# Kernel tuning notes

Measured on AMD Instinct MI355X. Metric: run time of the kernel, lower is better.

The kernel has to match this reference:

```python
import jax, jax.numpy as jnp
import numpy as np

N_NODES = 50000
N_EDGES = 800000
F_IN = 64
F_OUT = 64


def setup_inputs() -> dict:
    key = jax.random.key(0)
    k1, k2, k3, k4, k5 = jax.random.split(key, 5)
    x = jax.random.normal(k1, (N_NODES, F_IN), dtype=jnp.float32)
    edge_index = jax.random.randint(k2, (2, N_EDGES), 0, N_NODES, dtype=jnp.int32)
    # PyG GraphConv params: lin_rel (with bias) applied to aggregated neighbors,
    # lin_root (no bias) applied to the node's own features.
    scale = 1.0 / np.sqrt(F_IN)
    W_rel = jax.random.uniform(k3, (F_OUT, F_IN), dtype=jnp.float32, minval=-scale, maxval=scale)
    b_rel = jax.random.uniform(k4, (F_OUT,), dtype=jnp.float32, minval=-scale, maxval=scale)
    W_root = jax.random.uniform(k5, (F_OUT, F_IN), dtype=jnp.float32, minval=-scale, maxval=scale)
    return {"x": x, "W_rel": W_rel, "b_rel": b_rel, "W_root": W_root, "edge_index": edge_index}


def reference(x, W_rel, b_rel, W_root, edge_index):
    # GraphConv (aggr='add'): out = lin_rel(sum_{j in N(i)} x_j) + lin_root(x_i), then ReLU
    src, dst = edge_index[0], edge_index[1]
    # gather neighbor features along edges, scatter-add into destination nodes
    agg = jax.ops.segment_sum(x[src], dst, num_segments=x.shape[0])  # [N, F_IN]
    out = agg @ W_rel.T + b_rel + x @ W_root.T  # [N, F_OUT]
    return jax.nn.relu(out)
```

## Files before the change

kernel.cpp:

```cpp
#include <hip/hip_runtime.h>


#define FEAT 64
#define TNODES 64
#define TCAP 2048
#define KPAD 65
#define CSTR 16
#define TMAX 1024
#define GBIN 256

__global__ __launch_bounds__(256) void gcv2_prep(
    const float* __restrict__ W_rel, const float* __restrict__ W_root,
    float* __restrict__ WTrel, float* __restrict__ WTroot,
    int* __restrict__ tcnt, int n_cnt) {
  const int idx = blockIdx.x * 256 + threadIdx.x;
  if (idx < FEAT * FEAT) {
    const int o = idx >> 6, k = idx & 63;
    WTrel[k * FEAT + o] = W_rel[idx];
    WTroot[k * FEAT + o] = W_root[idx];
  }
  for (int i = idx; i < n_cnt; i += gridDim.x * 256) tcnt[i] = 0;
}

__global__ __launch_bounds__(256) void gcv2_bin(
    const int* __restrict__ eidx, int* __restrict__ tcnt,
    unsigned* __restrict__ tbuf, int n_edges, int n_tiles) {
  __shared__ int bh[TMAX];
  __shared__ int bbase[TMAX];

  const int t = threadIdx.x;
  for (int i = t; i < n_tiles; i += 256) bh[i] = 0;
  __syncthreads();

  const int per = (n_edges + gridDim.x - 1) / gridDim.x;
  const int e0 = blockIdx.x * per;
  const int e1 = min(e0 + per, n_edges);

  for (int e = e0 + t; e < e1; e += 256)
    atomicAdd(&bh[eidx[n_edges + e] >> 6], 1);
  __syncthreads();

  for (int i = t; i < n_tiles; i += 256) {
    const int c = bh[i];
    bbase[i] = (c > 0) ? atomicAdd(&tcnt[i * CSTR], c) : 0;
    bh[i] = 0;
  }
  __syncthreads();

  for (int e = e0 + t; e < e1; e += 256) {
    const int s = eidx[e];
    const int d = eidx[n_edges + e];
    const int tl = d >> 6;
    const int p = bbase[tl] + atomicAdd(&bh[tl], 1);
    if (p < TCAP)
      tbuf[(size_t)tl * TCAP + p] = ((unsigned)d << 16) | (unsigned)s;
  }
}

__global__ __launch_bounds__(256) void gcv2_main(
    const float* __restrict__ x,
    const float* __restrict__ WTrel,
    const float* __restrict__ b_rel,
    const float* __restrict__ WTroot,
    const int* __restrict__ tcnt,
    const unsigned* __restrict__ tbuf,
    float* __restrict__ out, int n_nodes) {
  __shared__ float aggT[FEAT * KPAD];
  __shared__ float xT[FEAT * KPAD];
  __shared__ unsigned short srcs[TCAP + 64];
  __shared__ int sh[TNODES];
  __shared__ int soff[TNODES + 1];
  __shared__ int scur[TNODES];

  const int t = threadIdx.x;
  const int lane = t & 63;
  const int w = t >> 6;
  const int tile = blockIdx.x;
  const int node0 = tile * TNODES;
  const int cnt = min(tcnt[tile * CSTR], TCAP);
  const unsigned* lst = tbuf + (size_t)tile * TCAP;

  if (t < TNODES) sh[t] = 0;
  if (t < 64 && cnt + t < TCAP + 64) srcs[cnt + t] = 0;
  {
    const int c4 = t & 15;
    const int rr = t >> 4;
#pragma unroll
    for (int p = 0; p < 4; ++p) {
      const int r = p * 16 + rr;
      const int gi = node0 + r;
      float4 v = make_float4(0.f, 0.f, 0.f, 0.f);
      if (gi < n_nodes) v = *(const float4*)(x + (size_t)gi * FEAT + c4 * 4);
      xT[(c4 * 4 + 0) * KPAD + r] = v.x;
      xT[(c4 * 4 + 1) * KPAD + r] = v.y;
      xT[(c4 * 4 + 2) * KPAD + r] = v.z;
      xT[(c4 * 4 + 3) * KPAD + r] = v.w;
    }
  }
  __syncthreads();

  for (int i = t; i < cnt; i += 256) atomicAdd(&sh[(lst[i] >> 16) & 63], 1);
  __syncthreads();

  if (w == 0) {
    int v = sh[lane];
    int s = v;
#pragma unroll
    for (int d = 1; d < 64; d <<= 1) {
      int u = __shfl_up(s, d, 64);
      if (lane >= d) s += u;
    }
    soff[lane] = s - v;
    scur[lane] = s - v;
    if (lane == 63) soff[64] = s;
  }
  __syncthreads();

  for (int i = t; i < cnt; i += 256) {
    const unsigned e = lst[i];
    const int d = (int)((e >> 16) & 63);
    srcs[atomicAdd(&scur[d], 1)] = (unsigned short)(e & 0xFFFFu);
  }
  __syncthreads();

  const int slot = lane >> 4;
  const int fq = lane & 15;
  for (int nn = 0; nn < 16; ++nn) {
    const int d = w * 16 + nn;
    const int jb = soff[d];
    const int je = soff[d + 1];
    float4 acc = make_float4(0.f, 0.f, 0.f, 0.f);
    const int i0 = slot, i1 = 4 + slot, i2 = 8 + slot, i3 = 12 + slot;
    for (int e0 = jb; e0 < je; e0 += 16) {
      const int m = je - e0;
      const int j0 = (i0 < m) ? e0 + i0 : cnt;
      const int j1 = (i1 < m) ? e0 + i1 : cnt;
      const int j2 = (i2 < m) ? e0 + i2 : cnt;
      const int j3 = (i3 < m) ? e0 + i3 : cnt;
      const int s0 = (int)srcs[j0];
      const int s1 = (int)srcs[j1];
      const int s2 = (int)srcs[j2];
      const int s3 = (int)srcs[j3];
      const float4 f0 = *(const float4*)(x + (size_t)s0 * FEAT + fq * 4);
      const float4 f1 = *(const float4*)(x + (size_t)s1 * FEAT + fq * 4);
      const float4 f2 = *(const float4*)(x + (size_t)s2 * FEAT + fq * 4);
      const float4 f3 = *(const float4*)(x + (size_t)s3 * FEAT + fq * 4);
      acc.x += (i0 < m ? f0.x : 0.f); acc.y += (i0 < m ? f0.y : 0.f);
      acc.z += (i0 < m ? f0.z : 0.f); acc.w += (i0 < m ? f0.w : 0.f);
      acc.x += (i1 < m ? f1.x : 0.f); acc.y += (i1 < m ? f1.y : 0.f);
      acc.z += (i1 < m ? f1.z : 0.f); acc.w += (i1 < m ? f1.w : 0.f);
      acc.x += (i2 < m ? f2.x : 0.f); acc.y += (i2 < m ? f2.y : 0.f);
      acc.z += (i2 < m ? f2.z : 0.f); acc.w += (i2 < m ? f2.w : 0.f);
      acc.x += (i3 < m ? f3.x : 0.f); acc.y += (i3 < m ? f3.y : 0.f);
      acc.z += (i3 < m ? f3.z : 0.f); acc.w += (i3 < m ? f3.w : 0.f);
    }
    acc.x += __shfl_xor(acc.x, 16, 64); acc.y += __shfl_xor(acc.y, 16, 64);
    acc.z += __shfl_xor(acc.z, 16, 64); acc.w += __shfl_xor(acc.w, 16, 64);
    acc.x += __shfl_xor(acc.x, 32, 64); acc.y += __shfl_xor(acc.y, 32, 64);
    acc.z += __shfl_xor(acc.z, 32, 64); acc.w += __shfl_xor(acc.w, 32, 64);
    if (slot == 0) {
      aggT[(fq * 4 + 0) * KPAD + d] = acc.x;
      aggT[(fq * 4 + 1) * KPAD + d] = acc.y;
      aggT[(fq * 4 + 2) * KPAD + d] = acc.z;
      aggT[(fq * 4 + 3) * KPAD + d] = acc.w;
    }
  }
  __syncthreads();

  const int oq = t & 15, rq = t >> 4;
  const int o0 = oq * 4, r0 = rq * 4;
  const float4 bias = *(const float4*)(b_rel + o0);
  float acc[4][4];
#pragma unroll
  for (int ri = 0; ri < 4; ++ri) {
    acc[ri][0] = bias.x; acc[ri][1] = bias.y;
    acc[ri][2] = bias.z; acc[ri][3] = bias.w;
  }
#pragma unroll 4
  for (int k = 0; k < FEAT; ++k) {
    const float4 wr = *(const float4*)(WTrel + k * FEAT + o0);
    const float4 wo = *(const float4*)(WTroot + k * FEAT + o0);
    const float a0 = aggT[k * KPAD + r0 + 0], a1 = aggT[k * KPAD + r0 + 1];
    const float a2 = aggT[k * KPAD + r0 + 2], a3 = aggT[k * KPAD + r0 + 3];
    const float x0 = xT[k * KPAD + r0 + 0], x1 = xT[k * KPAD + r0 + 1];
    const float x2 = xT[k * KPAD + r0 + 2], x3 = xT[k * KPAD + r0 + 3];
    acc[0][0] += a0 * wr.x + x0 * wo.x; acc[0][1] += a0 * wr.y + x0 * wo.y;
    acc[0][2] += a0 * wr.z + x0 * wo.z; acc[0][3] += a0 * wr.w + x0 * wo.w;
    acc[1][0] += a1 * wr.x + x1 * wo.x; acc[1][1] += a1 * wr.y + x1 * wo.y;
    acc[1][2] += a1 * wr.z + x1 * wo.z; acc[1][3] += a1 * wr.w + x1 * wo.w;
    acc[2][0] += a2 * wr.x + x2 * wo.x; acc[2][1] += a2 * wr.y + x2 * wo.y;
    acc[2][2] += a2 * wr.z + x2 * wo.z; acc[2][3] += a2 * wr.w + x2 * wo.w;
    acc[3][0] += a3 * wr.x + x3 * wo.x; acc[3][1] += a3 * wr.y + x3 * wo.y;
    acc[3][2] += a3 * wr.z + x3 * wo.z; acc[3][3] += a3 * wr.w + x3 * wo.w;
  }
#pragma unroll
  for (int ri = 0; ri < 4; ++ri) {
    const int gi = node0 + r0 + ri;
    if (gi < n_nodes) {
      float4 o4;
      o4.x = fmaxf(acc[ri][0], 0.f); o4.y = fmaxf(acc[ri][1], 0.f);
      o4.z = fmaxf(acc[ri][2], 0.f); o4.w = fmaxf(acc[ri][3], 0.f);
      *(float4*)(out + (size_t)gi * FEAT + o0) = o4;
    }
  }
}

extern "C" void kernel_launch(void* const* d_in, const int* in_sizes, int n_in,
                              void* d_out, int out_size, void* d_ws, size_t ws_size,
                              hipStream_t stream) {
  const float* x      = (const float*)d_in[0];
  const float* W_rel  = (const float*)d_in[1];
  const float* b_rel  = (const float*)d_in[2];
  const float* W_root = (const float*)d_in[3];
  const int* eidx     = (const int*)d_in[4];

  const int n_nodes = in_sizes[0] / FEAT;
  const int n_edges = in_sizes[4] / 2;
  const int n_tiles = (n_nodes + TNODES - 1) / TNODES;

  int* tcnt      = (int*)d_ws;
  unsigned* tbuf = (unsigned*)(tcnt + (size_t)n_tiles * CSTR);
  float* WTrel   = (float*)(tbuf + (size_t)n_tiles * TCAP);
  float* WTroot  = WTrel + FEAT * FEAT;

  float* out = (float*)d_out;

  const int n_cnt = n_tiles * CSTR;
  const int gPrep = (n_cnt + 255) / 256;
  gcv2_prep<<<gPrep, 256, 0, stream>>>(W_rel, W_root, WTrel, WTroot, tcnt,
                                       n_cnt);

  gcv2_bin<<<GBIN, 256, 0, stream>>>(eidx, tcnt, tbuf, n_edges, n_tiles);

  gcv2_main<<<n_tiles, 256, 0, stream>>>(x, WTrel, b_rel, WTroot, tcnt, tbuf,
                                         out, n_nodes);
}
```

Before: 142.9 us.

## Software-pipeline neighbor gather over 32-edge chunk descriptors with double buffering

The per-node serial gather loop is replaced by a per-wave list of 32-edge chunk descriptors, built with a wave prefix scan. Gathers are issued for the next chunk before the current one is reduced, with two register buffers of eight float4 loads each. The goal is to keep more global loads in flight and hide gather latency across node boundaries. aggT is now zeroed and accumulated with +=, and launch bounds request 3 blocks per CU. The costs are higher register pressure, wasted masked loads when degrees are well under 32, and a fixed descriptor capacity per wave (CCAP).

```diff
diff --git a/kernel.cpp b/kernel.cpp
--- a/kernel.cpp
+++ b/kernel.cpp
@@ -8,6 +8,7 @@
 #define CSTR 16
 #define TMAX 1024
 #define GBIN 256
+#define CCAP 96
 
 __global__ __launch_bounds__(256) void gcv2_prep(
     const float* __restrict__ W_rel, const float* __restrict__ W_root,
@@ -57,7 +58,7 @@
   }
 }
 
-__global__ __launch_bounds__(256) void gcv2_main(
+__global__ __launch_bounds__(256, 3) void gcv2_main(
     const float* __restrict__ x,
     const float* __restrict__ WTrel,
     const float* __restrict__ b_rel,
@@ -71,6 +72,8 @@
   __shared__ int sh[TNODES];
   __shared__ int soff[TNODES + 1];
   __shared__ int scur[TNODES];
+  __shared__ int cdesc[4 * CCAP];
+  __shared__ int ncK[4];
 
   const int t = threadIdx.x;
   const int lane = t & 63;
@@ -82,6 +85,7 @@
 
   if (t < TNODES) sh[t] = 0;
   if (t < 64 && cnt + t < TCAP + 64) srcs[cnt + t] = 0;
+  for (int i = t; i < FEAT * KPAD; i += 256) aggT[i] = 0.f;
   {
     const int c4 = t & 15;
     const int rr = t >> 4;
@@ -116,6 +120,29 @@
   }
   __syncthreads();
 
+  {
+    int myc = 0, jb0 = 0;
+    const int nd = w * 16 + (lane & 15);
+    if (lane < 16) {
+      jb0 = soff[nd];
+      const int deg = soff[nd + 1] - jb0;
+      myc = (deg + 31) >> 5;
+    }
+    int sc = myc;
+#pragma unroll
+    for (int dlt = 1; dlt < 16; dlt <<= 1) {
+      const int u = __shfl_up(sc, dlt, 16);
+      if ((lane & 15) >= dlt) sc += u;
+    }
+    const int pos = sc - myc;
+    const int tot = __shfl(sc, 15, 64);
+    if (lane == 0) ncK[w] = tot;
+    if (lane < 16) {
+      for (int c = 0; c < myc; ++c)
+        cdesc[w * CCAP + pos + c] = (nd << 16) | (jb0 + c * 32);
+    }
+  }
+
   for (int i = t; i < cnt; i += 256) {
     const unsigned e = lst[i];
     const int d = (int)((e >> 16) & 63);
@@ -125,44 +152,110 @@
 
   const int slot = lane >> 4;
   const int fq = lane & 15;
-  for (int nn = 0; nn < 16; ++nn) {
-    const int d = w * 16 + nn;
-    const int jb = soff[d];
-    const int je = soff[d + 1];
-    float4 acc = make_float4(0.f, 0.f, 0.f, 0.f);
-    const int i0 = slot, i1 = 4 + slot, i2 = 8 + slot, i3 = 12 + slot;
-    for (int e0 = jb; e0 < je; e0 += 16) {
-      const int m = je - e0;
-      const int j0 = (i0 < m) ? e0 + i0 : cnt;
-      const int j1 = (i1 < m) ? e0 + i1 : cnt;
-      const int j2 = (i2 < m) ? e0 + i2 : cnt;
-      const int j3 = (i3 < m) ? e0 + i3 : cnt;
-      const int s0 = (int)srcs[j0];
-      const int s1 = (int)srcs[j1];
-      const int s2 = (int)srcs[j2];
-      const int s3 = (int)srcs[j3];
-      const float4 f0 = *(const float4*)(x + (size_t)s0 * FEAT + fq * 4);
-      const float4 f1 = *(const float4*)(x + (size_t)s1 * FEAT + fq * 4);
-      const float4 f2 = *(const float4*)(x + (size_t)s2 * FEAT + fq * 4);
-      const float4 f3 = *(const float4*)(x + (size_t)s3 * FEAT + fq * 4);
-      acc.x += (i0 < m ? f0.x : 0.f); acc.y += (i0 < m ? f0.y : 0.f);
-      acc.z += (i0 < m ? f0.z : 0.f); acc.w += (i0 < m ? f0.w : 0.f);
-      acc.x += (i1 < m ? f1.x : 0.f); acc.y += (i1 < m ? f1.y : 0.f);
-      acc.z += (i1 < m ? f1.z : 0.f); acc.w += (i1 < m ? f1.w : 0.f);
-      acc.x += (i2 < m ? f2.x : 0.f); acc.y += (i2 < m ? f2.y : 0.f);
-      acc.z += (i2 < m ? f2.z : 0.f); acc.w += (i2 < m ? f2.w : 0.f);
-      acc.x += (i3 < m ? f3.x : 0.f); acc.y += (i3 < m ? f3.y : 0.f);
-      acc.z += (i3 < m ? f3.z : 0.f); acc.w += (i3 < m ? f3.w : 0.f);
-    }
-    acc.x += __shfl_xor(acc.x, 16, 64); acc.y += __shfl_xor(acc.y, 16, 64);
-    acc.z += __shfl_xor(acc.z, 16, 64); acc.w += __shfl_xor(acc.w, 16, 64);
-    acc.x += __shfl_xor(acc.x, 32, 64); acc.y += __shfl_xor(acc.y, 32, 64);
-    acc.z += __shfl_xor(acc.z, 32, 64); acc.w += __shfl_xor(acc.w, 32, 64);
-    if (slot == 0) {
-      aggT[(fq * 4 + 0) * KPAD + d] = acc.x;
-      aggT[(fq * 4 + 1) * KPAD + d] = acc.y;
-      aggT[(fq * 4 + 2) * KPAD + d] = acc.z;
-      aggT[(fq * 4 + 3) * KPAD + d] = acc.w;
+  const int nc = ncK[w];
+  const int cbase = w * CCAP;
+
+#define GC_ISSUE(DSC, F0, F1, F2, F3, F4, F5, F6, F7)                        \
+  {                                                                          \
+    const int e0_ = (DSC) & 0xFFFF;                                          \
+    const int je_ = soff[((DSC) >> 16) + 1];                                 \
+    const int m_ = je_ - e0_;                                                \
+    const int j0_ = (slot < m_) ? e0_ + slot : cnt;                          \
+    const int j1_ = (4 + slot < m_) ? e0_ + 4 + slot : cnt;                  \
+    const int j2_ = (8 + slot < m_) ? e0_ + 8 + slot : cnt;                  \
+    const int j3_ = (12 + slot < m_) ? e0_ + 12 + slot : cnt;                \
+    const int j4_ = (16 + slot < m_) ? e0_ + 16 + slot : cnt;                \
+    const int j5_ = (20 + slot < m_) ? e0_ + 20 + slot : cnt;                \
+    const int j6_ = (24 + slot < m_) ? e0_ + 24 + slot : cnt;                \
+    const int j7_ = (28 + slot < m_) ? e0_ + 28 + slot : cnt;                \
+    const int s0_ = (int)srcs[j0_];                                          \
+    const int s1_ = (int)srcs[j1_];                                          \
+    const int s2_ = (int)srcs[j2_];                                          \
+    const int s3_ = (int)srcs[j3_];                                          \
+    const int s4_ = (int)srcs[j4_];                                          \
+    const int s5_ = (int)srcs[j5_];                                          \
+    const int s6_ = (int)srcs[j6_];                                          \
+    const int s7_ = (int)srcs[j7_];                                          \
+    F0 = *(const float4*)(x + (size_t)s0_ * FEAT + fq * 4);                  \
+    F1 = *(const float4*)(x + (size_t)s1_ * FEAT + fq * 4);                  \
+    F2 = *(const float4*)(x + (size_t)s2_ * FEAT + fq * 4);                  \
+    F3 = *(const float4*)(x + (size_t)s3_ * FEAT + fq * 4);                  \
+    F4 = *(const float4*)(x + (size_t)s4_ * FEAT + fq * 4);                  \
+    F5 = *(const float4*)(x + (size_t)s5_ * FEAT + fq * 4);                  \
+    F6 = *(const float4*)(x + (size_t)s6_ * FEAT + fq * 4);                  \
+    F7 = *(const float4*)(x + (size_t)s7_ * FEAT + fq * 4);                  \
+  }
+
+#define GC_CONSUME(DSC, F0, F1, F2, F3, F4, F5, F6, F7)                      \
+  {                                                                          \
+    const int d_ = (DSC) >> 16;                                              \
+    const int e0_ = (DSC) & 0xFFFF;                                          \
+    const int m_ = soff[d_ + 1] - e0_;                                       \
+    float4 acc = make_float4(0.f, 0.f, 0.f, 0.f);                            \
+    acc.x += (slot < m_ ? F0.x : 0.f); acc.y += (slot < m_ ? F0.y : 0.f);    \
+    acc.z += (slot < m_ ? F0.z : 0.f); acc.w += (slot < m_ ? F0.w : 0.f);    \
+    acc.x += (4 + slot < m_ ? F1.x : 0.f);                                   \
+    acc.y += (4 + slot < m_ ? F1.y : 0.f);                                   \
+    acc.z += (4 + slot < m_ ? F1.z : 0.f);                                   \
+    acc.w += (4 + slot < m_ ? F1.w : 0.f);                                   \
+    acc.x += (8 + slot < m_ ? F2.x : 0.f);                                   \
+    acc.y += (8 + slot < m_ ? F2.y : 0.f);                                   \
+    acc.z += (8 + slot < m_ ? F2.z : 0.f);                                   \
+    acc.w += (8 + slot < m_ ? F2.w : 0.f);                                   \
+    acc.x += (12 + slot < m_ ? F3.x : 0.f);                                  \
+    acc.y += (12 + slot < m_ ? F3.y : 0.f);                                  \
+    acc.z += (12 + slot < m_ ? F3.z : 0.f);                                  \
+    acc.w += (12 + slot < m_ ? F3.w : 0.f);                                  \
+    acc.x += (16 + slot < m_ ? F4.x : 0.f);                                  \
+    acc.y += (16 + slot < m_ ? F4.y : 0.f);                                  \
+    acc.z += (16 + slot < m_ ? F4.z : 0.f);                                  \
+    acc.w += (16 + slot < m_ ? F4.w : 0.f);                                  \
+    acc.x += (20 + slot < m_ ? F5.x : 0.f);                                  \
+    acc.y += (20 + slot < m_ ? F5.y : 0.f);                                  \
+    acc.z += (20 + slot < m_ ? F5.z : 0.f);                                  \
+    acc.w += (20 + slot < m_ ? F5.w : 0.f);                                  \
+    acc.x += (24 + slot < m_ ? F6.x : 0.f);                                  \
+    acc.y += (24 + slot < m_ ? F6.y : 0.f);                                  \
+    acc.z += (24 + slot < m_ ? F6.z : 0.f);                                  \
+    acc.w += (24 + slot < m_ ? F6.w : 0.f);                                  \
+    acc.x += (28 + slot < m_ ? F7.x : 0.f);                                  \
+    acc.y += (28 + slot < m_ ? F7.y : 0.f);                                  \
+    acc.z += (28 + slot < m_ ? F7.z : 0.f);                                  \
+    acc.w += (28 + slot < m_ ? F7.w : 0.f);                                  \
+    acc.x += __shfl_xor(acc.x, 16, 64); acc.y += __shfl_xor(acc.y, 16, 64);  \
+    acc.z += __shfl_xor(acc.z, 16, 64); acc.w += __shfl_xor(acc.w, 16, 64);  \
+    acc.x += __shfl_xor(acc.x, 32, 64); acc.y += __shfl_xor(acc.y, 32, 64);  \
+    acc.z += __shfl_xor(acc.z, 32, 64); acc.w += __shfl_xor(acc.w, 32, 64);  \
+    if (slot == 0) {                                                         \
+      aggT[(fq * 4 + 0) * KPAD + d_] += acc.x;                               \
+      aggT[(fq * 4 + 1) * KPAD + d_] += acc.y;                               \
+      aggT[(fq * 4 + 2) * KPAD + d_] += acc.z;                               \
+      aggT[(fq * 4 + 3) * KPAD + d_] += acc.w;                               \
+    }                                                                        \
+  }
+
+  {
+    int descA = 0, descB = 0;
+    float4 fA0, fA1, fA2, fA3, fA4, fA5, fA6, fA7;
+    float4 fB0, fB1, fB2, fB3, fB4, fB5, fB6, fB7;
+    if (nc > 0) {
+      descA = cdesc[cbase];
+      GC_ISSUE(descA, fA0, fA1, fA2, fA3, fA4, fA5, fA6, fA7);
+    }
+    for (int j = 0; j < nc; j += 2) {
+      const bool hasB = (j + 1 < nc);
+      if (hasB) {
+        descB = cdesc[cbase + j + 1];
+        GC_ISSUE(descB, fB0, fB1, fB2, fB3, fB4, fB5, fB6, fB7);
+      }
+      GC_CONSUME(descA, fA0, fA1, fA2, fA3, fA4, fA5, fA6, fA7);
+      if (hasB) {
+        if (j + 2 < nc) {
+          descA = cdesc[cbase + j + 2];
+          GC_ISSUE(descA, fA0, fA1, fA2, fA3, fA4, fA5, fA6, fA7);
+        }
+        GC_CONSUME(descB, fB0, fB1, fB2, fB3, fB4, fB5, fB6, fB7);
+      }
     }
   }
   __syncthreads();
```

After: 148.0 us. 3.5% more time.

## Stream neighbor features into LDS via async ring and scatter with LDS atomics

Applied to the files above, without the earlier changes.

Drops the in-block counting sort (histogram, prefix scan, reorder) of each tile's edges. Neighbor feature rows are instead fetched with global_load_lds into a 3-slot per-wave LDS ring and scatter-added into the transposed aggregate with LDS float atomics. The goal is to overlap gather latency with accumulation and remove several barriers and sort passes. The costs are one LDS atomic per edge-feature element, more LDS per block, and reliance on manual vmcnt waits being enough to order ring-slot reuse.

```diff
diff --git a/kernel.cpp b/kernel.cpp
--- a/kernel.cpp
+++ b/kernel.cpp
@@ -8,6 +8,7 @@
 #define CSTR 16
 #define TMAX 1024
 #define GBIN 256
+#define RING 3
 
 __global__ __launch_bounds__(256) void gcv2_prep(
     const float* __restrict__ W_rel, const float* __restrict__ W_root,
@@ -57,7 +58,13 @@
   }
 }
 
-__global__ __launch_bounds__(256) void gcv2_main(
+__device__ __forceinline__ void load_lds16(const float* g, float* l) {
+  __builtin_amdgcn_global_load_lds(
+      (const __attribute__((address_space(1))) unsigned*)g,
+      (__attribute__((address_space(3))) unsigned*)l, 16, 0, 0);
+}
+
+__global__ __launch_bounds__(256, 3) void gcv2_main(
     const float* __restrict__ x,
     const float* __restrict__ WTrel,
     const float* __restrict__ b_rel,
@@ -67,10 +74,9 @@
     float* __restrict__ out, int n_nodes) {
   __shared__ float aggT[FEAT * KPAD];
   __shared__ float xT[FEAT * KPAD];
-  __shared__ unsigned short srcs[TCAP + 64];
-  __shared__ int sh[TNODES];
-  __shared__ int soff[TNODES + 1];
-  __shared__ int scur[TNODES];
+  __shared__ unsigned short srcL[TCAP];
+  __shared__ unsigned char dstL[TCAP];
+  __shared__ float stg[4][RING][256];
 
   const int t = threadIdx.x;
   const int lane = t & 63;
@@ -79,9 +85,14 @@
   const int node0 = tile * TNODES;
   const int cnt = min(tcnt[tile * CSTR], TCAP);
   const unsigned* lst = tbuf + (size_t)tile * TCAP;
-
-  if (t < TNODES) sh[t] = 0;
-  if (t < 64 && cnt + t < TCAP + 64) srcs[cnt + t] = 0;
+  const int cnt_pad = (cnt + 15) & ~15;
+
+  for (int i = t; i < FEAT * KPAD; i += 256) aggT[i] = 0.f;
+  for (int i = t; i < cnt_pad; i += 256) {
+    const unsigned e = (i < cnt) ? lst[i] : 0u;
+    srcL[i] = (unsigned short)(e & 0xFFFFu);
+    dstL[i] = (i < cnt) ? (unsigned char)((e >> 16) & 63) : (unsigned char)64;
+  }
   {
     const int c4 = t & 15;
     const int rr = t >> 4;
@@ -99,71 +110,56 @@
   }
   __syncthreads();
 
-  for (int i = t; i < cnt; i += 256) atomicAdd(&sh[(lst[i] >> 16) & 63], 1);
-  __syncthreads();
-
-  if (w == 0) {
-    int v = sh[lane];
-    int s = v;
-#pragma unroll
-    for (int d = 1; d < 64; d <<= 1) {
-      int u = __shfl_up(s, d, 64);
-      if (lane >= d) s += u;
+  {
+    const int f = lane;
+    const int nb = cnt_pad >> 2;
+    const int nbw = (nb > w) ? ((nb - w + 3) >> 2) : 0;
+    const int aggbase = f * KPAD;
+    const int jj = lane >> 4;
+    const int ch = lane & 15;
+
+#define DMA_ISSUE(Q, S)                                                   \
+  {                                                                       \
+    const int b_ = w + ((Q) << 2);                                        \
+    const unsigned s_ = srcL[(b_ << 2) + jj];                             \
+    load_lds16(x + ((size_t)s_ << 6) + (ch << 2), &stg[w][S][0]);         \
+  }
+
+#define REDUCE(Q, S)                                                      \
+  {                                                                       \
+    const int b_ = w + ((Q) << 2);                                        \
+    const unsigned dp_ = *(const unsigned*)&dstL[b_ << 2];                \
+    const float* sp_ = &stg[w][S][0];                                     \
+    const float v0_ = sp_[f];                                             \
+    const float v1_ = sp_[64 + f];                                        \
+    const float v2_ = sp_[128 + f];                                       \
+    const float v3_ = sp_[192 + f];                                       \
+    atomicAdd(&aggT[aggbase + (int)(dp_ & 255u)], v0_);                   \
+    atomicAdd(&aggT[aggbase + (int)((dp_ >> 8) & 255u)], v1_);            \
+    atomicAdd(&aggT[aggbase + (int)((dp_ >> 16) & 255u)], v2_);           \
+    atomicAdd(&aggT[aggbase + (int)(dp_ >> 24)], v3_);                    \
+  }
+
+    if (nbw > 0) {
+      DMA_ISSUE(0, 0);
+      if (nbw > 1) DMA_ISSUE(1, 1);
+      if (nbw > 2) DMA_ISSUE(2, 2);
+      int s = 0;
+      for (int q = 0; q < nbw; ++q) {
+        if (q + RING < nbw) {
+          asm volatile("s_waitcnt vmcnt(2)" ::: "memory");
+        } else {
+          asm volatile("s_waitcnt vmcnt(0)" ::: "memory");
+        }
+        __builtin_amdgcn_sched_barrier(0);
+        REDUCE(q, s);
+        __builtin_amdgcn_sched_barrier(0);
+        if (q + RING < nbw) DMA_ISSUE(q + RING, s);
+        s = (s == RING - 1) ? 0 : s + 1;
+      }
     }
-    soff[lane] = s - v;
-    scur[lane] = s - v;
-    if (lane == 63) soff[64] = s;
-  }
-  __syncthreads();
-
-  for (int i = t; i < cnt; i += 256) {
-    const unsigned e = lst[i];
-    const int d = (int)((e >> 16) & 63);
-    srcs[atomicAdd(&scur[d], 1)] = (unsigned short)(e & 0xFFFFu);
-  }
-  __syncthreads();
-
-  const int slot = lane >> 4;
-  const int fq = lane & 15;
-  for (int nn = 0; nn < 16; ++nn) {
-    const int d = w * 16 + nn;
-    const int jb = soff[d];
-    const int je = soff[d + 1];
-    float4 acc = make_float4(0.f, 0.f, 0.f, 0.f);
-    const int i0 = slot, i1 = 4 + slot, i2 = 8 + slot, i3 = 12 + slot;
-    for (int e0 = jb; e0 < je; e0 += 16) {
-      const int m = je - e0;
-      const int j0 = (i0 < m) ? e0 + i0 : cnt;
-      const int j1 = (i1 < m) ? e0 + i1 : cnt;
-      const int j2 = (i2 < m) ? e0 + i2 : cnt;
-      const int j3 = (i3 < m) ? e0 + i3 : cnt;
-      const int s0 = (int)srcs[j0];
-      const int s1 = (int)srcs[j1];
-      const int s2 = (int)srcs[j2];
-      const int s3 = (int)srcs[j3];
-      const float4 f0 = *(const float4*)(x + (size_t)s0 * FEAT + fq * 4);
-      const float4 f1 = *(const float4*)(x + (size_t)s1 * FEAT + fq * 4);
-      const float4 f2 = *(const float4*)(x + (size_t)s2 * FEAT + fq * 4);
-      const float4 f3 = *(const float4*)(x + (size_t)s3 * FEAT + fq * 4);
-      acc.x += (i0 < m ? f0.x : 0.f); acc.y += (i0 < m ? f0.y : 0.f);
-      acc.z += (i0 < m ? f0.z : 0.f); acc.w += (i0 < m ? f0.w : 0.f);
-      acc.x += (i1 < m ? f1.x : 0.f); acc.y += (i1 < m ? f1.y : 0.f);
-      acc.z += (i1 < m ? f1.z : 0.f); acc.w += (i1 < m ? f1.w : 0.f);
-      acc.x += (i2 < m ? f2.x : 0.f); acc.y += (i2 < m ? f2.y : 0.f);
-      acc.z += (i2 < m ? f2.z : 0.f); acc.w += (i2 < m ? f2.w : 0.f);
-      acc.x += (i3 < m ? f3.x : 0.f); acc.y += (i3 < m ? f3.y : 0.f);
-      acc.z += (i3 < m ? f3.z : 0.f); acc.w += (i3 < m ? f3.w : 0.f);
-    }
-    acc.x += __shfl_xor(acc.x, 16, 64); acc.y += __shfl_xor(acc.y, 16, 64);
-    acc.z += __shfl_xor(acc.z, 16, 64); acc.w += __shfl_xor(acc.w, 16, 64);
-    acc.x += __shfl_xor(acc.x, 32, 64); acc.y += __shfl_xor(acc.y, 32, 64);
-    acc.z += __shfl_xor(acc.z, 32, 64); acc.w += __shfl_xor(acc.w, 32, 64);
-    if (slot == 0) {
-      aggT[(fq * 4 + 0) * KPAD + d] = acc.x;
-      aggT[(fq * 4 + 1) * KPAD + d] = acc.y;
-      aggT[(fq * 4 + 2) * KPAD + d] = acc.z;
-      aggT[(fq * 4 + 3) * KPAD + d] = acc.w;
-    }
+#undef DMA_ISSUE
+#undef REDUCE
   }
   __syncthreads();
 
```

Measured after the change: 465.7 us. 3.26x slower.
